# Performance work log

Measured on AMD Instinct MI355X. Metric: run time of the kernel, lower is better.

Reference implementation:

```python
import jax, jax.numpy as jnp
import numpy as np

D = 1024      # d_model
H = 16        # n_heads
HD = D // H   # head_dim = 64
SQ = 1024     # seq_len_q
SKV = 1024    # seq_len_kv
B = 4
MAXL = max(SQ, SKV)  # max_len of relative positional encoding
SCALE = 1.0 / np.sqrt(HD).astype(np.float32)


def setup_inputs() -> dict:
    key = jax.random.key(0)
    ks = jax.random.split(key, 8)
    s = 0.02
    return {
        "query": jax.random.normal(ks[0], (B, SQ, D), dtype=jnp.float32),
        "key_value": jax.random.normal(ks[1], (B, SKV, D), dtype=jnp.float32),
        "Wq": jax.random.normal(ks[2], (D, D), dtype=jnp.float32) * s,
        "bq": jnp.zeros((D,), dtype=jnp.float32),
        "Wk": jax.random.normal(ks[3], (D, D), dtype=jnp.float32) * s,
        "bk": jnp.zeros((D,), dtype=jnp.float32),
        "Wv": jax.random.normal(ks[4], (D, D), dtype=jnp.float32) * s,
        "bv": jnp.zeros((D,), dtype=jnp.float32),
        "Wo": jax.random.normal(ks[5], (D, D), dtype=jnp.float32) * s,
        "bo": jnp.zeros((D,), dtype=jnp.float32),
        # nn.Parameter(torch.randn(2*max_len-1, head_dim))
        "rel_table": jax.random.normal(ks[6], (2 * MAXL - 1, HD), dtype=jnp.float32),
    }


def reference(query, key_value, Wq, bq, Wk, bk, Wv, bv, Wo, bo, rel_table):
    b = query.shape[0]
    q = query.reshape(b, SQ, D)
    kv = key_value.reshape(b, SKV, D)
    # projections, then split heads -> [b, H, S, HD]
    Q = (q @ Wq + bq).reshape(b, SQ, H, HD).transpose(0, 2, 1, 3)
    K = (kv @ Wk + bk).reshape(b, SKV, H, HD).transpose(0, 2, 1, 3)
    V = (kv @ Wv + bv).reshape(b, SKV, H, HD).transpose(0, 2, 1, 3)
    # content scores
    scores = jnp.einsum('bhid,bhjd->bhij', Q, K) * SCALE
    # relative position bias: rel_pos[i,j] = clip(i-j+MAXL-1, 0, 2*MAXL-2)
    i = jnp.arange(SQ)[:, None]
    j = jnp.arange(SKV)[None, :]
    idx = jnp.clip(i - j + MAXL - 1, 0, 2 * MAXL - 2)
    rel = rel_table[idx]  # [SQ, SKV, HD]
    scores = scores + jnp.einsum('bhid,ijd->bhij', Q, rel)
    attn = jax.nn.softmax(scores, axis=-1)  # dropout is identity in eval
    out = jnp.einsum('bhij,bhjd->bhid', attn, V)
    out = out.transpose(0, 2, 1, 3).reshape(b, SQ, D)
    out = out @ Wo + bo
    return out.reshape(b, -1)
```

## Files before the change

### kernel.cpp

```cpp
#include <hip/hip_runtime.h>
#include <hip/hip_bf16.h>
#include <stdint.h>


typedef __attribute__((ext_vector_type(8))) short short8;
typedef __attribute__((ext_vector_type(4))) float f32x4;

constexpr int Bz = 4, SQv = 1024, SKVv = 1024, Dv = 1024, Hv = 16, HDv = 64;
constexpr float SCALEv = 0.125f;

constexpr size_t OFF_QB  = 0;
constexpr size_t OFF_KVB = 8388608;
constexpr size_t OFF_WQT = 16777216;
constexpr size_t OFF_WKT = 18874368;
constexpr size_t OFF_WVT = 20971520;
constexpr size_t OFF_WOT = 23068672;
constexpr size_t OFF_REL = 25165824;
constexpr size_t OFF_Q   = 25427968;
constexpr size_t OFF_K   = 33816576;
constexpr size_t OFF_V   = 42205184;
constexpr size_t OFF_AO  = 50593792;

__device__ __forceinline__ unsigned short f2bf(float f) {
  union { float f; unsigned int u; } v; v.f = f;
  unsigned int r = (v.u + 0x7fffu + ((v.u >> 16) & 1u)) >> 16;
  return (unsigned short)r;
}

__device__ __forceinline__ void gload_lds16(const unsigned short* g, unsigned short* l) {
  __builtin_amdgcn_global_load_lds(
      (const __attribute__((address_space(1))) unsigned int*)g,
      (__attribute__((address_space(3))) unsigned int*)l, 16, 0, 0);
}

template <int CTRL>
__device__ __forceinline__ float dpp_ror(float v) {
  int x = __builtin_amdgcn_update_dpp(__builtin_bit_cast(int, v),
                                      __builtin_bit_cast(int, v),
                                      CTRL, 0xf, 0xf, false);
  return __builtin_bit_cast(float, x);
}
__device__ __forceinline__ float red16_max(float v) {
  v = fmaxf(v, dpp_ror<0x121>(v));
  v = fmaxf(v, dpp_ror<0x122>(v));
  v = fmaxf(v, dpp_ror<0x124>(v));
  v = fmaxf(v, dpp_ror<0x128>(v));
  return v;
}
__device__ __forceinline__ float red16_sum(float v) {
  v += dpp_ror<0x121>(v);
  v += dpp_ror<0x122>(v);
  v += dpp_ror<0x124>(v);
  v += dpp_ror<0x128>(v);
  return v;
}

__global__ __launch_bounds__(256) void k_prep(const float* __restrict__ q,
                                              const float* __restrict__ kv,
                                              const float* __restrict__ rel,
                                              const float* __restrict__ Wq,
                                              const float* __restrict__ Wk,
                                              const float* __restrict__ Wv,
                                              const float* __restrict__ Wo,
                                              unsigned short* __restrict__ qb,
                                              unsigned short* __restrict__ kvb,
                                              unsigned short* __restrict__ relb,
                                              unsigned short* __restrict__ Wqt,
                                              unsigned short* __restrict__ Wkt,
                                              unsigned short* __restrict__ Wvt,
                                              unsigned short* __restrict__ Wot) {
  __shared__ unsigned short t[64][72];
  const int bx = blockIdx.x;
  if (bx < 4096) {
    const float* s = bx < 2048 ? q : kv;
    unsigned short* d = bx < 2048 ? qb : kvb;
    const int base = (bx & 2047) * 2048 + threadIdx.x * 8;
    float4 f0 = *(const float4*)(s + base);
    float4 f1 = *(const float4*)(s + base + 4);
    unsigned short o[8] = {f2bf(f0.x), f2bf(f0.y), f2bf(f0.z), f2bf(f0.w),
                           f2bf(f1.x), f2bf(f1.y), f2bf(f1.z), f2bf(f1.w)};
    *(uint4*)(d + base) = *(const uint4*)o;
    return;
  }
  if (bx < 4160) {
    const int i = (bx - 4096) * 2048 + threadIdx.x * 8;
    const int nsrc = 2047 * 64;
    unsigned short o[8];
    if (i + 8 <= nsrc) {
      float4 f0 = *(const float4*)(rel + i);
      float4 f1 = *(const float4*)(rel + i + 4);
      o[0]=f2bf(f0.x); o[1]=f2bf(f0.y); o[2]=f2bf(f0.z); o[3]=f2bf(f0.w);
      o[4]=f2bf(f1.x); o[5]=f2bf(f1.y); o[6]=f2bf(f1.z); o[7]=f2bf(f1.w);
    } else {
#pragma unroll
      for (int k = 0; k < 8; k++) o[k] = (i + k < nsrc) ? f2bf(rel[i + k]) : (unsigned short)0;
    }
    *(uint4*)(relb + i) = *(const uint4*)o;
    return;
  }
  const int tt = bx - 4160;
  const int z = tt >> 8, tile = tt & 255;
  const float* W = z == 0 ? Wq : z == 1 ? Wk : z == 2 ? Wv : Wo;
  unsigned short* Wt = z == 0 ? Wqt : z == 1 ? Wkt : z == 2 ? Wvt : Wot;
  const int r0 = (tile >> 4) * 64, c0 = (tile & 15) * 64;
  const int tid = threadIdx.x;
  const int r = tid >> 2, cc = (tid & 3) * 16;
  const float* src = W + (size_t)(r0 + r) * Dv + c0 + cc;
#pragma unroll
  for (int i = 0; i < 16; i += 4) {
    float4 f = *(const float4*)(src + i);
    t[r][cc + i + 0] = f2bf(f.x);
    t[r][cc + i + 1] = f2bf(f.y);
    t[r][cc + i + 2] = f2bf(f.z);
    t[r][cc + i + 3] = f2bf(f.w);
  }
  __syncthreads();
  unsigned short tmp[16];
#pragma unroll
  for (int i = 0; i < 16; i++) tmp[i] = t[cc + i][r];
  unsigned short* dstp = Wt + (size_t)(c0 + r) * Dv + r0 + cc;
  *(uint4*)(dstp)     = *(const uint4*)&tmp[0];
  *((uint4*)dstp + 1) = *(const uint4*)&tmp[8];
}

__global__ __launch_bounds__(256) void k_gemm3(const unsigned short* __restrict__ qb,
                                               const unsigned short* __restrict__ kvb,
                                               const unsigned short* __restrict__ Wqt,
                                               const unsigned short* __restrict__ Wkt,
                                               const unsigned short* __restrict__ Wvt,
                                               const float* __restrict__ bq,
                                               const float* __restrict__ bk,
                                               const float* __restrict__ bv,
                                               unsigned short* __restrict__ Qb,
                                               unsigned short* __restrict__ Kb,
                                               unsigned short* __restrict__ Vtb) {
  __shared__ unsigned short As[128 * 32];
  __shared__ unsigned short Bs[128 * 32];
  const int z = blockIdx.z;
  const unsigned short* A  = z == 0 ? qb : kvb;
  const unsigned short* Bt = z == 0 ? Wqt : z == 1 ? Wkt : Wvt;
  const float* bias        = z == 0 ? bq : z == 1 ? bk : bv;
  unsigned short* Cout     = z == 0 ? Qb : z == 1 ? Kb : Vtb;
  const int K = Dv, N = Dv;

  const int tid = threadIdx.x;
  const int l = tid & 63, w = tid >> 6;
  const int wr = w >> 1, wc = w & 1;
  const int m0 = blockIdx.y * 128, n0 = blockIdx.x * 128;
  const int lr = l & 15, kk = (l >> 4) * 8;
  const int srow = tid >> 2, soff = (tid & 3) * 8;

  const unsigned short* Ag = A + (size_t)(m0 + srow) * K + soff;
  const unsigned short* Bg = Bt + (size_t)(n0 + srow) * K + soff;
  unsigned short* AsD = &As[tid * 8];
  unsigned short* BsD = &Bs[tid * 8];

  f32x4 acc[4][4] = {};

  for (int k0 = 0; k0 < K; k0 += 32) {
    __syncthreads();
    gload_lds16(Ag + k0, AsD);
    gload_lds16(Ag + (size_t)64 * K + k0, AsD + 2048);
    gload_lds16(Bg + k0, BsD);
    gload_lds16(Bg + (size_t)64 * K + k0, BsD + 2048);
    __syncthreads();
    short8 af[4], bf[4];
#pragma unroll
    for (int m = 0; m < 4; m++) af[m] = *(const short8*)&As[(wr * 64 + m * 16 + lr) * 32 + kk];
#pragma unroll
    for (int n = 0; n < 4; n++) bf[n] = *(const short8*)&Bs[(wc * 64 + n * 16 + lr) * 32 + kk];
    __builtin_amdgcn_s_setprio(1);
#pragma unroll
    for (int m = 0; m < 4; m++)
#pragma unroll
      for (int n = 0; n < 4; n++)
        acc[m][n] = __builtin_amdgcn_mfma_f32_16x16x32_bf16(af[m], bf[n], acc[m][n], 0, 0, 0);
    __builtin_amdgcn_s_setprio(0);
  }

#pragma unroll
  for (int m = 0; m < 4; m++) {
    const int row_base = m0 + wr * 64 + m * 16 + (l >> 4) * 4;
#pragma unroll
    for (int n = 0; n < 4; n++) {
      const int col = n0 + wc * 64 + n * 16 + lr;
      const float bv4 = bias[col];
      if (z == 2) {
        const int h = col >> 6, hd = col & 63;
        const int bb = row_base >> 10, j = row_base & 1023;
        unsigned short t4[4];
#pragma unroll
        for (int r = 0; r < 4; r++) t4[r] = f2bf(acc[m][n][r] + bv4);
        *(uint2*)&Cout[((size_t)((bb * 16 + h) * 64 + hd)) * 1024 + j] = *(const uint2*)t4;
      } else {
#pragma unroll
        for (int r = 0; r < 4; r++)
          Cout[(size_t)(row_base + r) * N + col] = f2bf(acc[m][n][r] + bv4);
      }
    }
  }
}

__global__ __launch_bounds__(256) void k_gemmO(const unsigned short* __restrict__ A,
                                               const unsigned short* __restrict__ Bt,
                                               const float* __restrict__ bias,
                                               float* __restrict__ Cout) {
  __shared__ unsigned short As[64 * 32];
  __shared__ unsigned short Bs[128 * 32];
  const int K = Dv, N = Dv;
  const int tid = threadIdx.x;
  const int l = tid & 63, w = tid >> 6;
  const int wr = w >> 1, wc = w & 1;
  const int m0 = blockIdx.y * 64, n0 = blockIdx.x * 128;
  const int lr = l & 15, kk = (l >> 4) * 8;
  const int srow = tid >> 2, soff = (tid & 3) * 8;

  const unsigned short* Ag = A + (size_t)(m0 + srow) * K + soff;
  const unsigned short* Bg = Bt + (size_t)(n0 + srow) * K + soff;
  unsigned short* AsD = &As[tid * 8];
  unsigned short* BsD = &Bs[tid * 8];

  f32x4 acc[2][4] = {};

  for (int k0 = 0; k0 < K; k0 += 32) {
    __syncthreads();
    gload_lds16(Ag + k0, AsD);
    gload_lds16(Bg + k0, BsD);
    gload_lds16(Bg + (size_t)64 * K + k0, BsD + 2048);
    __syncthreads();
    short8 af[2], bf[4];
#pragma unroll
    for (int m = 0; m < 2; m++) af[m] = *(const short8*)&As[(wr * 32 + m * 16 + lr) * 32 + kk];
#pragma unroll
    for (int n = 0; n < 4; n++) bf[n] = *(const short8*)&Bs[(wc * 64 + n * 16 + lr) * 32 + kk];
    __builtin_amdgcn_s_setprio(1);
#pragma unroll
    for (int m = 0; m < 2; m++)
#pragma unroll
      for (int n = 0; n < 4; n++)
        acc[m][n] = __builtin_amdgcn_mfma_f32_16x16x32_bf16(af[m], bf[n], acc[m][n], 0, 0, 0);
    __builtin_amdgcn_s_setprio(0);
  }

#pragma unroll
  for (int m = 0; m < 2; m++) {
    const int row_base = m0 + wr * 32 + m * 16 + (l >> 4) * 4;
#pragma unroll
    for (int n = 0; n < 4; n++) {
      const int col = n0 + wc * 64 + n * 16 + lr;
      const float bv4 = bias[col];
#pragma unroll
      for (int r = 0; r < 4; r++)
        Cout[(size_t)(row_base + r) * N + col] = acc[m][n][r] + bv4;
    }
  }
}

__global__ __launch_bounds__(256) void k_attn(const unsigned short* __restrict__ Qb,
                                              const unsigned short* __restrict__ Kb,
                                              const unsigned short* __restrict__ Vt,
                                              const unsigned short* __restrict__ relb,
                                              unsigned short* __restrict__ AO) {
  __shared__ unsigned short Ks[2][64][68];
  __shared__ unsigned short Vs[2][64][68];
  __shared__ float Ts[4][16][66];
  __shared__ unsigned short Ps[4][16][68];

  const int tid = threadIdx.x, l = tid & 63, w = tid >> 6;
  const int lr = l & 15, lg = l >> 4, kk = lg * 8;
  const int i0 = blockIdx.x * 64;
  const int h = blockIdx.y;
  const int b = blockIdx.z;

  const unsigned short* Kg  = Kb + (size_t)b * SKVv * Dv + h * HDv;
  const unsigned short* Vtg = Vt + ((size_t)(b * Hv + h) * HDv) * (size_t)SKVv;

  const unsigned short* Qg = Qb + ((size_t)(b * SQv + i0 + w * 16 + lr)) * Dv + h * HDv;
  short8 aq0 = *(const short8*)&Qg[kk];
  short8 aq1 = *(const short8*)&Qg[32 + kk];

  const int sr = tid >> 2, sc = (tid & 3) * 16;

  uint4 pk0, pk1, pv0, pv1;
  auto ldnext = [&](int j0) {
    pk0 = *(const uint4*)&Kg[(size_t)(j0 + sr) * Dv + sc];
    pk1 = *(const uint4*)&Kg[(size_t)(j0 + sr) * Dv + sc + 8];
    pv0 = *(const uint4*)&Vtg[(size_t)sr * SKVv + j0 + sc];
    pv1 = *(const uint4*)&Vtg[(size_t)sr * SKVv + j0 + sc + 8];
  };
  auto wrbuf = [&](int buf) {
    *(uint4*)&Ks[buf][sr][sc]     = pk0;
    *(uint4*)&Ks[buf][sr][sc + 8] = pk1;
    *(uint4*)&Vs[buf][sr][sc]     = pv0;
    *(uint4*)&Vs[buf][sr][sc + 8] = pv1;
  };

  ldnext(0);
  wrbuf(0);
  __syncthreads();

  f32x4 Oacc[4] = {};
  float mrow[4], lrow[4];
#pragma unroll
  for (int r = 0; r < 4; r++) { mrow[r] = -1e30f; lrow[r] = 0.f; }

  for (int it = 0; it < 16; ++it) {
    const int cur = it & 1;
    const int j0 = it * 64;
    if (it < 15) ldnext(j0 + 64);

    const int base = i0 - j0 + 960 + w * 16;
    short8 br0[5], br1[5];
#pragma unroll
    for (int tf = 0; tf < 5; tf++) {
      const unsigned short* rp = &relb[(size_t)(base + tf * 16 + lr) * HDv];
      br0[tf] = *(const short8*)&rp[kk];
      br1[tf] = *(const short8*)&rp[32 + kk];
    }

    __builtin_amdgcn_s_setprio(1);
    f32x4 sacc[4] = {};
#pragma unroll
    for (int jf = 0; jf < 4; jf++) {
      short8 bk0 = *(const short8*)&Ks[cur][jf * 16 + lr][kk];
      short8 bk1 = *(const short8*)&Ks[cur][jf * 16 + lr][32 + kk];
      sacc[jf] = __builtin_amdgcn_mfma_f32_16x16x32_bf16(aq0, bk0, sacc[jf], 0, 0, 0);
      sacc[jf] = __builtin_amdgcn_mfma_f32_16x16x32_bf16(aq1, bk1, sacc[jf], 0, 0, 0);
    }

#pragma unroll
    for (int tf = 0; tf < 5; tf++) {
      f32x4 tacc = {};
      tacc = __builtin_amdgcn_mfma_f32_16x16x32_bf16(aq0, br0[tf], tacc, 0, 0, 0);
      tacc = __builtin_amdgcn_mfma_f32_16x16x32_bf16(aq1, br1[tf], tacc, 0, 0, 0);
#pragma unroll
      for (int r = 0; r < 4; r++) {
        const int col = (lg * 4 + r) - (tf * 16 + lr) + 63;
        if ((unsigned)col < 64u) Ts[w][lg * 4 + r][col] = tacc[r];
      }
    }
    __builtin_amdgcn_s_setprio(0);

    float p[4][4];
#pragma unroll
    for (int r = 0; r < 4; r++) {
      const int rr = lg * 4 + r;
#pragma unroll
      for (int jf = 0; jf < 4; jf++)
        p[jf][r] = sacc[jf][r] * SCALEv + Ts[w][rr][jf * 16 + lr];
      float mx = fmaxf(fmaxf(p[0][r], p[1][r]), fmaxf(p[2][r], p[3][r]));
      mx = red16_max(mx);
      const float mnew = fmaxf(mrow[r], mx);
      const float resc = __expf(mrow[r] - mnew);
      mrow[r] = mnew;
      float s = 0.f;
#pragma unroll
      for (int jf = 0; jf < 4; jf++) {
        p[jf][r] = __expf(p[jf][r] - mnew);
        s += p[jf][r];
      }
      s = red16_sum(s);
      lrow[r] = lrow[r] * resc + s;
#pragma unroll
      for (int df = 0; df < 4; df++) Oacc[df][r] *= resc;
#pragma unroll
      for (int jf = 0; jf < 4; jf++) Ps[w][rr][jf * 16 + lr] = f2bf(p[jf][r]);
    }

    short8 ap0 = *(const short8*)&Ps[w][lr][kk];
    short8 ap1 = *(const short8*)&Ps[w][lr][32 + kk];
    __builtin_amdgcn_s_setprio(1);
#pragma unroll
    for (int df = 0; df < 4; df++) {
      short8 bv0 = *(const short8*)&Vs[cur][df * 16 + lr][kk];
      short8 bv1 = *(const short8*)&Vs[cur][df * 16 + lr][32 + kk];
      Oacc[df] = __builtin_amdgcn_mfma_f32_16x16x32_bf16(ap0, bv0, Oacc[df], 0, 0, 0);
      Oacc[df] = __builtin_amdgcn_mfma_f32_16x16x32_bf16(ap1, bv1, Oacc[df], 0, 0, 0);
    }
    __builtin_amdgcn_s_setprio(0);

    if (it < 15) wrbuf(cur ^ 1);
    __syncthreads();
  }

#pragma unroll
  for (int r = 0; r < 4; r++) {
    const float inv = 1.f / lrow[r];
    const size_t row = (size_t)(b * SQv + i0 + w * 16 + lg * 4 + r) * Dv + h * HDv;
#pragma unroll
    for (int df = 0; df < 4; df++)
      AO[row + df * 16 + lr] = f2bf(Oacc[df][r] * inv);
  }
}

extern "C" void kernel_launch(void* const* d_in, const int* in_sizes, int n_in,
                              void* d_out, int out_size, void* d_ws, size_t ws_size,
                              hipStream_t stream) {
  const float* query = (const float*)d_in[0];
  const float* keyv  = (const float*)d_in[1];
  const float* Wq    = (const float*)d_in[2];
  const float* bq    = (const float*)d_in[3];
  const float* Wk    = (const float*)d_in[4];
  const float* bk    = (const float*)d_in[5];
  const float* Wv    = (const float*)d_in[6];
  const float* bv    = (const float*)d_in[7];
  const float* Wo    = (const float*)d_in[8];
  const float* bo    = (const float*)d_in[9];
  const float* rel   = (const float*)d_in[10];

  char* ws = (char*)d_ws;
  unsigned short* qb   = (unsigned short*)(ws + OFF_QB);
  unsigned short* kvb  = (unsigned short*)(ws + OFF_KVB);
  unsigned short* Wqt  = (unsigned short*)(ws + OFF_WQT);
  unsigned short* Wkt  = (unsigned short*)(ws + OFF_WKT);
  unsigned short* Wvt  = (unsigned short*)(ws + OFF_WVT);
  unsigned short* Wot  = (unsigned short*)(ws + OFF_WOT);
  unsigned short* relb = (unsigned short*)(ws + OFF_REL);
  unsigned short* Qb   = (unsigned short*)(ws + OFF_Q);
  unsigned short* Kb   = (unsigned short*)(ws + OFF_K);
  unsigned short* Vtb  = (unsigned short*)(ws + OFF_V);
  unsigned short* AOb  = (unsigned short*)(ws + OFF_AO);

  k_prep<<<5184, 256, 0, stream>>>(query, keyv, rel, Wq, Wk, Wv, Wo,
                                   qb, kvb, relb, Wqt, Wkt, Wvt, Wot);

  dim3 g3(Dv / 128, (Bz * SQv) / 128, 3);
  k_gemm3<<<g3, 256, 0, stream>>>(qb, kvb, Wqt, Wkt, Wvt, bq, bk, bv, Qb, Kb, Vtb);

  dim3 ga(SQv / 64, Hv, Bz);
  k_attn<<<ga, 256, 0, stream>>>(Qb, Kb, Vtb, relb, AOb);

  dim3 go(Dv / 128, (Bz * SQv) / 64);
  k_gemmO<<<go, 256, 0, stream>>>(AOb, Wot, bo, (float*)d_out);
}
```

Measured before the change: 184.7 us.

## Read K/V directly from global in attention, remap blocks, lazy softmax rescale

Removes the shared-memory double-buffered K/V staging and the per-tile block barrier, so each wave loads K and V fragments straight from global memory (relying on L2/cache reuse). The grid becomes 1D with a swizzled block-to-work mapping intended to spread or co-locate blocks across XCDs, and a launch-bounds occupancy hint is added. The online softmax now skips rescaling unless the row max grows by more than a threshold, which saves exp and multiply work but lets exponentials grow up to e^8 before renormalising. The trade-off is more redundant global/L2 traffic, since the four waves each fetch the same K/V tiles.

```diff
diff --git a/kernel.cpp b/kernel.cpp
--- a/kernel.cpp
+++ b/kernel.cpp
@@ -256,21 +256,22 @@
   }
 }
 
-__global__ __launch_bounds__(256) void k_attn(const unsigned short* __restrict__ Qb,
-                                              const unsigned short* __restrict__ Kb,
-                                              const unsigned short* __restrict__ Vt,
-                                              const unsigned short* __restrict__ relb,
-                                              unsigned short* __restrict__ AO) {
-  __shared__ unsigned short Ks[2][64][68];
-  __shared__ unsigned short Vs[2][64][68];
+__global__ __launch_bounds__(256, 5) void k_attn(const unsigned short* __restrict__ Qb,
+                                                 const unsigned short* __restrict__ Kb,
+                                                 const unsigned short* __restrict__ Vt,
+                                                 const unsigned short* __restrict__ relb,
+                                                 unsigned short* __restrict__ AO) {
   __shared__ float Ts[4][16][66];
   __shared__ unsigned short Ps[4][16][68];
 
   const int tid = threadIdx.x, l = tid & 63, w = tid >> 6;
   const int lr = l & 15, lg = l >> 4, kk = lg * 8;
-  const int i0 = blockIdx.x * 64;
-  const int h = blockIdx.y;
-  const int b = blockIdx.z;
+
+  const int raw = blockIdx.x;
+  const int work = (raw & 7) * 128 + (raw >> 3);
+  const int i0 = (work & 15) * 64;
+  const int h = (work >> 4) & 15;
+  const int b = work >> 8;
 
   const unsigned short* Kg  = Kb + (size_t)b * SKVv * Dv + h * HDv;
   const unsigned short* Vtg = Vt + ((size_t)(b * Hv + h) * HDv) * (size_t)SKVv;
@@ -279,60 +280,34 @@
   short8 aq0 = *(const short8*)&Qg[kk];
   short8 aq1 = *(const short8*)&Qg[32 + kk];
 
-  const int sr = tid >> 2, sc = (tid & 3) * 16;
-
-  uint4 pk0, pk1, pv0, pv1;
-  auto ldnext = [&](int j0) {
-    pk0 = *(const uint4*)&Kg[(size_t)(j0 + sr) * Dv + sc];
-    pk1 = *(const uint4*)&Kg[(size_t)(j0 + sr) * Dv + sc + 8];
-    pv0 = *(const uint4*)&Vtg[(size_t)sr * SKVv + j0 + sc];
-    pv1 = *(const uint4*)&Vtg[(size_t)sr * SKVv + j0 + sc + 8];
-  };
-  auto wrbuf = [&](int buf) {
-    *(uint4*)&Ks[buf][sr][sc]     = pk0;
-    *(uint4*)&Ks[buf][sr][sc + 8] = pk1;
-    *(uint4*)&Vs[buf][sr][sc]     = pv0;
-    *(uint4*)&Vs[buf][sr][sc + 8] = pv1;
-  };
-
-  ldnext(0);
-  wrbuf(0);
-  __syncthreads();
-
   f32x4 Oacc[4] = {};
   float mrow[4], lrow[4];
 #pragma unroll
   for (int r = 0; r < 4; r++) { mrow[r] = -1e30f; lrow[r] = 0.f; }
 
   for (int it = 0; it < 16; ++it) {
-    const int cur = it & 1;
     const int j0 = it * 64;
-    if (it < 15) ldnext(j0 + 64);
+
+    __builtin_amdgcn_s_setprio(1);
+    f32x4 sacc[4] = {};
+#pragma unroll
+    for (int jf = 0; jf < 4; jf++) {
+      const unsigned short* kp = &Kg[(size_t)(j0 + jf * 16 + lr) * Dv];
+      short8 bk0 = *(const short8*)&kp[kk];
+      short8 bk1 = *(const short8*)&kp[32 + kk];
+      sacc[jf] = __builtin_amdgcn_mfma_f32_16x16x32_bf16(aq0, bk0, sacc[jf], 0, 0, 0);
+      sacc[jf] = __builtin_amdgcn_mfma_f32_16x16x32_bf16(aq1, bk1, sacc[jf], 0, 0, 0);
+    }
 
     const int base = i0 - j0 + 960 + w * 16;
-    short8 br0[5], br1[5];
 #pragma unroll
     for (int tf = 0; tf < 5; tf++) {
       const unsigned short* rp = &relb[(size_t)(base + tf * 16 + lr) * HDv];
-      br0[tf] = *(const short8*)&rp[kk];
-      br1[tf] = *(const short8*)&rp[32 + kk];
-    }
-
-    __builtin_amdgcn_s_setprio(1);
-    f32x4 sacc[4] = {};
-#pragma unroll
-    for (int jf = 0; jf < 4; jf++) {
-      short8 bk0 = *(const short8*)&Ks[cur][jf * 16 + lr][kk];
-      short8 bk1 = *(const short8*)&Ks[cur][jf * 16 + lr][32 + kk];
-      sacc[jf] = __builtin_amdgcn_mfma_f32_16x16x32_bf16(aq0, bk0, sacc[jf], 0, 0, 0);
-      sacc[jf] = __builtin_amdgcn_mfma_f32_16x16x32_bf16(aq1, bk1, sacc[jf], 0, 0, 0);
-    }
-
-#pragma unroll
-    for (int tf = 0; tf < 5; tf++) {
+      short8 br0 = *(const short8*)&rp[kk];
+      short8 br1 = *(const short8*)&rp[32 + kk];
       f32x4 tacc = {};
-      tacc = __builtin_amdgcn_mfma_f32_16x16x32_bf16(aq0, br0[tf], tacc, 0, 0, 0);
-      tacc = __builtin_amdgcn_mfma_f32_16x16x32_bf16(aq1, br1[tf], tacc, 0, 0, 0);
+      tacc = __builtin_amdgcn_mfma_f32_16x16x32_bf16(aq0, br0, tacc, 0, 0, 0);
+      tacc = __builtin_amdgcn_mfma_f32_16x16x32_bf16(aq1, br1, tacc, 0, 0, 0);
 #pragma unroll
       for (int r = 0; r < 4; r++) {
         const int col = (lg * 4 + r) - (tf * 16 + lr) + 63;
@@ -341,7 +316,7 @@
     }
     __builtin_amdgcn_s_setprio(0);
 
-    float p[4][4];
+    float p[4][4], mx4[4];
 #pragma unroll
     for (int r = 0; r < 4; r++) {
       const int rr = lg * 4 + r;
@@ -349,20 +324,33 @@
       for (int jf = 0; jf < 4; jf++)
         p[jf][r] = sacc[jf][r] * SCALEv + Ts[w][rr][jf * 16 + lr];
       float mx = fmaxf(fmaxf(p[0][r], p[1][r]), fmaxf(p[2][r], p[3][r]));
-      mx = red16_max(mx);
-      const float mnew = fmaxf(mrow[r], mx);
-      const float resc = __expf(mrow[r] - mnew);
-      mrow[r] = mnew;
+      mx4[r] = red16_max(mx);
+    }
+    bool grow = false;
+#pragma unroll
+    for (int r = 0; r < 4; r++) grow = grow || (mx4[r] > mrow[r] + 8.0f);
+    if (__any(grow ? 1 : 0)) {
+#pragma unroll
+      for (int r = 0; r < 4; r++) {
+        const float mnew = fmaxf(mrow[r], mx4[r]);
+        const float resc = __expf(mrow[r] - mnew);
+        mrow[r] = mnew;
+        lrow[r] *= resc;
+#pragma unroll
+        for (int df = 0; df < 4; df++) Oacc[df][r] *= resc;
+      }
+    }
+#pragma unroll
+    for (int r = 0; r < 4; r++) {
+      const int rr = lg * 4 + r;
       float s = 0.f;
 #pragma unroll
       for (int jf = 0; jf < 4; jf++) {
-        p[jf][r] = __expf(p[jf][r] - mnew);
+        p[jf][r] = __expf(p[jf][r] - mrow[r]);
         s += p[jf][r];
       }
       s = red16_sum(s);
-      lrow[r] = lrow[r] * resc + s;
-#pragma unroll
-      for (int df = 0; df < 4; df++) Oacc[df][r] *= resc;
+      lrow[r] += s;
 #pragma unroll
       for (int jf = 0; jf < 4; jf++) Ps[w][rr][jf * 16 + lr] = f2bf(p[jf][r]);
     }
@@ -372,15 +360,13 @@
     __builtin_amdgcn_s_setprio(1);
 #pragma unroll
     for (int df = 0; df < 4; df++) {
-      short8 bv0 = *(const short8*)&Vs[cur][df * 16 + lr][kk];
-      short8 bv1 = *(const short8*)&Vs[cur][df * 16 + lr][32 + kk];
+      const unsigned short* vp = &Vtg[(size_t)(df * 16 + lr) * SKVv + j0];
+      short8 bv0 = *(const short8*)&vp[kk];
+      short8 bv1 = *(const short8*)&vp[32 + kk];
       Oacc[df] = __builtin_amdgcn_mfma_f32_16x16x32_bf16(ap0, bv0, Oacc[df], 0, 0, 0);
       Oacc[df] = __builtin_amdgcn_mfma_f32_16x16x32_bf16(ap1, bv1, Oacc[df], 0, 0, 0);
     }
     __builtin_amdgcn_s_setprio(0);
-
-    if (it < 15) wrbuf(cur ^ 1);
-    __syncthreads();
   }
 
 #pragma unroll
@@ -427,8 +413,7 @@
   dim3 g3(Dv / 128, (Bz * SQv) / 128, 3);
   k_gemm3<<<g3, 256, 0, stream>>>(qb, kvb, Wqt, Wkt, Wvt, bq, bk, bv, Qb, Kb, Vtb);
 
-  dim3 ga(SQv / 64, Hv, Bz);
-  k_attn<<<ga, 256, 0, stream>>>(Qb, Kb, Vtb, relb, AOb);
+  k_attn<<<1024, 256, 0, stream>>>(Qb, Kb, Vtb, relb, AOb);
 
   dim3 go(Dv / 128, (Bz * SQv) / 64);
   k_gemmO<<<go, 256, 0, stream>>>(AOb, Wot, bo, (float*)d_out);
```

Result: slower. 274.2 us (+48.4%).
